# Kernel optimization log

Hardware: AMD Instinct MI355X
Metric: run time of the kernel (lower is better)

## Reference

```python
import jax, jax.numpy as jnp
import numpy as np

D_MODEL = 2048
HEADS = 16
HEAD_DIM = D_MODEL // HEADS
INNER = 8192
SEQ = 2048
EPS = 1e-5


def _layernorm(x, g, b):
    mu = jnp.mean(x, axis=-1, keepdims=True)
    var = jnp.mean(jnp.square(x - mu), axis=-1, keepdims=True)
    return (x - mu) * jax.lax.rsqrt(var + EPS) * g + b


def setup_inputs() -> dict:
    key = jax.random.key(0)
    ks = jax.random.split(key, 10)
    s = 0.02
    return {
        "x": jax.random.normal(ks[0], (1, SEQ, D_MODEL), dtype=jnp.float32),
        "C_w": jax.random.normal(ks[1], (D_MODEL, 3 * D_MODEL), dtype=jnp.float32) * s,
        "C_b": jnp.zeros((3 * D_MODEL,), dtype=jnp.float32),
        "lin_w": jax.random.normal(ks[2], (D_MODEL, D_MODEL), dtype=jnp.float32) * s,
        "lin_b": jnp.zeros((D_MODEL,), dtype=jnp.float32),
        "ff1_w": jax.random.normal(ks[3], (D_MODEL, INNER), dtype=jnp.float32) * s,
        "ff1_b": jnp.zeros((INNER,), dtype=jnp.float32),
        "ff2_w": jax.random.normal(ks[4], (INNER, D_MODEL), dtype=jnp.float32) * s,
        "ff2_b": jnp.zeros((D_MODEL,), dtype=jnp.float32),
        "ln1_g": jnp.ones((D_MODEL,), dtype=jnp.float32),
        "ln1_b": jnp.zeros((D_MODEL,), dtype=jnp.float32),
        "ln2_g": jnp.ones((D_MODEL,), dtype=jnp.float32),
        "ln2_b": jnp.zeros((D_MODEL,), dtype=jnp.float32),
    }


def reference(x, C_w, C_b, lin_w, lin_b, ff1_w, ff1_b, ff2_w, ff2_b,
              ln1_g, ln1_b, ln2_g, ln2_b):
    b, s, d = x.shape
    c = x @ C_w + C_b                       # [b, s, 3d]
    q, k, v = jnp.split(c, 3, axis=2)
    q = q.reshape(b, s, HEADS, HEAD_DIM)
    k = k.reshape(b, s, HEADS, HEAD_DIM)
    v = v.reshape(b, s, HEADS, HEAD_DIM)
    # NOTE: source scales by sqrt(d_model), NOT sqrt(head_dim)
    qk = jnp.einsum('bqhd,bkhd->bhqk', q, k) / jnp.sqrt(jnp.float32(d))
    causal = jnp.tril(jnp.ones((s, s), dtype=bool))  # [s, s]
    qk = jnp.where(causal[None, None, :, :], qk, -jnp.inf)
    scores = jax.nn.softmax(qk, axis=3)
    out = jnp.einsum('bhqk,bkhd->bqhd', scores, v).reshape(b, s, d)
    attn = out @ lin_w + lin_b
    h1 = _layernorm(x + attn, ln1_g, ln1_b)
    ff = jax.nn.gelu(h1 @ ff1_w + ff1_b, approximate=False) @ ff2_w + ff2_b
    return _layernorm(h1 + ff, ln2_g, ln2_b)
```

## Files before the change

### kernel.cpp

```cpp
#include <hip/hip_runtime.h>
#include <hip/hip_bf16.h>

#define SEQ 2048
#define DM 2048
#define NH 16
#define HD 128
#define FF 8192

typedef float f4v __attribute__((ext_vector_type(4)));
typedef short s8v __attribute__((ext_vector_type(8)));

__device__ __forceinline__ ushort f2bf(float f) {
  unsigned int x = __float_as_uint(f);
  unsigned int r = (x + 0x7FFFu + ((x >> 16) & 1u)) >> 16;
  return (ushort)r;
}

#define AS1 __attribute__((address_space(1)))
#define AS3 __attribute__((address_space(3)))
__device__ __forceinline__ void load16_lds(const ushort* g, ushort* l) {
  __builtin_amdgcn_global_load_lds((const AS1 unsigned int*)g, (AS3 unsigned int*)l, 16, 0, 0);
}

__global__ __launch_bounds__(256) void k_cvt(const float* __restrict__ in,
                                             ushort* __restrict__ out, int n4) {
  int i = blockIdx.x * 256 + threadIdx.x;
  if (i >= n4) return;
  f4v v = reinterpret_cast<const f4v*>(in)[i];
  ushort4 u;
  u.x = f2bf(v[0]); u.y = f2bf(v[1]); u.z = f2bf(v[2]); u.w = f2bf(v[3]);
  reinterpret_cast<ushort4*>(out)[i] = u;
}

__global__ __launch_bounds__(256) void k_tr(const float* __restrict__ W,
                                            ushort* __restrict__ Wt,
                                            int K, int N) {
  __shared__ float tile[32][36];
  int t = threadIdx.x;
  int n0 = blockIdx.x * 32, k0 = blockIdx.y * 32;
  int lr = t >> 3, lc = (t & 7) * 4;
  *(f4v*)&tile[lr][lc] = *(const f4v*)&W[(size_t)(k0 + lr) * N + n0 + lc];
  __syncthreads();
  int sn = t >> 3, sk = (t & 7) * 4;
  ushort4 u;
  u.x = f2bf(tile[sk + 0][sn]);
  u.y = f2bf(tile[sk + 1][sn]);
  u.z = f2bf(tile[sk + 2][sn]);
  u.w = f2bf(tile[sk + 3][sn]);
  *(ushort4*)&Wt[(size_t)(n0 + sn) * K + k0 + sk] = u;
}

__global__ __launch_bounds__(256) void k_gemm(const ushort* __restrict__ A,
                                              const ushort* __restrict__ Bt,
                                              const float* __restrict__ bias,
                                              float* __restrict__ Cf,
                                              ushort* __restrict__ Cb,
                                              int M, int N, int K, int gelu) {
  __shared__ ushort As[128 * 64];
  __shared__ ushort Bs[128 * 64];
  const int m0 = blockIdx.y * 128, n0 = blockIdx.x * 128;
  const int t = threadIdx.x;
  const int wave = t >> 6, lane = t & 63;
  const int wm = (wave >> 1) * 64, wn = (wave & 1) * 64;
  const int quad = lane >> 4, l16 = lane & 15;
  f4v acc[4][4] = {};
  const int srow = lane >> 3;
  const int scg = (lane & 7) ^ srow;
  const ushort* gA = A + (size_t)(m0 + wave * 32 + srow) * K + scg * 8;
  const ushort* gB = Bt + (size_t)(n0 + wave * 32 + srow) * K + scg * 8;
  ushort* lA = &As[(wave * 32 + srow - srow) * 64];
  ushort* lB = &Bs[(wave * 32) * 64];
  lA = &As[(wave * 32) * 64];

  for (int k0 = 0; k0 < K; k0 += 64) {
#pragma unroll
    for (int p = 0; p < 4; ++p) {
      load16_lds(gA + (size_t)p * 8 * K + k0, lA + p * 8 * 64);
      load16_lds(gB + (size_t)p * 8 * K + k0, lB + p * 8 * 64);
    }
    __syncthreads();
#pragma unroll
    for (int kk = 0; kk < 64; kk += 32) {
      s8v af[4], bf[4];
#pragma unroll
      for (int i = 0; i < 4; ++i) {
        int ar = wm + i * 16 + l16;
        af[i] = *(const s8v*)&As[ar * 64 + ((((kk >> 3) + quad) ^ (ar & 7)) * 8)];
      }
#pragma unroll
      for (int j = 0; j < 4; ++j) {
        int br = wn + j * 16 + l16;
        bf[j] = *(const s8v*)&Bs[br * 64 + ((((kk >> 3) + quad) ^ (br & 7)) * 8)];
      }
#pragma unroll
      for (int i = 0; i < 4; ++i)
#pragma unroll
        for (int j = 0; j < 4; ++j)
          acc[i][j] = __builtin_amdgcn_mfma_f32_16x16x32_bf16(af[i], bf[j], acc[i][j], 0, 0, 0);
    }
    __syncthreads();
  }
#pragma unroll
  for (int i = 0; i < 4; ++i) {
    int rbase = m0 + wm + i * 16 + quad * 4;
#pragma unroll
    for (int j = 0; j < 4; ++j) {
      int cidx = n0 + wn + j * 16 + l16;
      float b = bias[cidx];
#pragma unroll
      for (int r = 0; r < 4; ++r) {
        float v = acc[i][j][r] + b;
        if (gelu) v = 0.5f * v * (1.0f + erff(v * 0.70710678118654752f));
        if (Cf) Cf[(size_t)(rbase + r) * N + cidx] = v;
        if (Cb) Cb[(size_t)(rbase + r) * N + cidx] = f2bf(v);
      }
    }
  }
}

__global__ __launch_bounds__(256) void k_attn_mfma(const ushort* __restrict__ qkv,
                                                   ushort* __restrict__ ctx) {
  __shared__ ushort Ks[64][136];
  __shared__ ushort Vt[128][72];
  __shared__ ushort Ps[4][16][72];
  const int idx = blockIdx.x;
  const int h = idx & (NH - 1);
  const int qt = (SEQ / 64 - 1) - (idx >> 4);
  const int q0 = qt * 64;
  const int t = threadIdx.x;
  const int wave = t >> 6, lane = t & 63;
  const int quad = lane >> 4, l16 = lane & 15;
  const float scale = 0.022097086912079608f;

  s8v aq[4];
  {
    const ushort* qp = qkv + (size_t)(q0 + 16 * wave + l16) * (3 * DM) + h * HD + quad * 8;
#pragma unroll
    for (int ks = 0; ks < 4; ++ks)
      aq[ks] = *(const s8v*)(qp + ks * 32);
  }
  f4v acc_o[8] = {};
  float m_r[4], l_r[4];
#pragma unroll
  for (int r = 0; r < 4; ++r) { m_r[r] = -1e30f; l_r[r] = 0.0f; }

  for (int kt = 0; kt <= qt; ++kt) {
    const int k0 = kt * 64;
    __syncthreads();
    {
      const ushort* kp = qkv + (size_t)k0 * (3 * DM) + DM + h * HD;
#pragma unroll
      for (int i = 0; i < 4; ++i) {
        int ch = t + i * 256;
        int row = ch >> 4, c8 = (ch & 15) * 8;
        *(s8v*)&Ks[row][c8] = *(const s8v*)(kp + (size_t)row * (3 * DM) + c8);
      }
      const ushort* vp = qkv + (size_t)k0 * (3 * DM) + 2 * DM + h * HD;
#pragma unroll
      for (int i = 0; i < 4; ++i) {
        int id = t + i * 256;
        int d = id & 127, sg = id >> 7;
        ushort e0 = vp[(size_t)(sg * 8 + 0) * (3 * DM) + d];
        ushort e1 = vp[(size_t)(sg * 8 + 1) * (3 * DM) + d];
        ushort e2 = vp[(size_t)(sg * 8 + 2) * (3 * DM) + d];
        ushort e3 = vp[(size_t)(sg * 8 + 3) * (3 * DM) + d];
        ushort e4 = vp[(size_t)(sg * 8 + 4) * (3 * DM) + d];
        ushort e5 = vp[(size_t)(sg * 8 + 5) * (3 * DM) + d];
        ushort e6 = vp[(size_t)(sg * 8 + 6) * (3 * DM) + d];
        ushort e7 = vp[(size_t)(sg * 8 + 7) * (3 * DM) + d];
        uint4 pk;
        pk.x = (uint)e0 | ((uint)e1 << 16);
        pk.y = (uint)e2 | ((uint)e3 << 16);
        pk.z = (uint)e4 | ((uint)e5 << 16);
        pk.w = (uint)e6 | ((uint)e7 << 16);
        *(uint4*)&Vt[d][sg * 8] = pk;
      }
    }
    __syncthreads();

    f4v sacc[4] = {};
#pragma unroll
    for (int ks = 0; ks < 4; ++ks) {
      s8v bk[4];
#pragma unroll
      for (int j = 0; j < 4; ++j)
        bk[j] = *(const s8v*)&Ks[j * 16 + l16][ks * 32 + quad * 8];
#pragma unroll
      for (int j = 0; j < 4; ++j)
        sacc[j] = __builtin_amdgcn_mfma_f32_16x16x32_bf16(aq[ks], bk[j], sacc[j], 0, 0, 0);
    }
    if (kt == qt) {
#pragma unroll
      for (int j = 0; j < 4; ++j)
#pragma unroll
        for (int r = 0; r < 4; ++r) {
          int lrow = 16 * wave + quad * 4 + r;
          int lcol = j * 16 + l16;
          sacc[j][r] = (lcol > lrow) ? -1e30f : sacc[j][r] * scale;
        }
    } else {
#pragma unroll
      for (int j = 0; j < 4; ++j)
#pragma unroll
        for (int r = 0; r < 4; ++r) sacc[j][r] *= scale;
    }
    float alpha[4];
#pragma unroll
    for (int r = 0; r < 4; ++r) {
      float mx = fmaxf(fmaxf(sacc[0][r], sacc[1][r]), fmaxf(sacc[2][r], sacc[3][r]));
      mx = fmaxf(mx, __shfl_xor(mx, 1));
      mx = fmaxf(mx, __shfl_xor(mx, 2));
      mx = fmaxf(mx, __shfl_xor(mx, 4));
      mx = fmaxf(mx, __shfl_xor(mx, 8));
      float mn = fmaxf(m_r[r], mx);
      alpha[r] = __expf(m_r[r] - mn);
      m_r[r] = mn;
      float ps = 0.0f;
#pragma unroll
      for (int j = 0; j < 4; ++j) {
        float p = __expf(sacc[j][r] - mn);
        sacc[j][r] = p;
        ps += p;
      }
      ps += __shfl_xor(ps, 1);
      ps += __shfl_xor(ps, 2);
      ps += __shfl_xor(ps, 4);
      ps += __shfl_xor(ps, 8);
      l_r[r] = l_r[r] * alpha[r] + ps;
    }
#pragma unroll
    for (int j = 0; j < 4; ++j)
#pragma unroll
      for (int r = 0; r < 4; ++r)
        Ps[wave][quad * 4 + r][j * 16 + l16] = f2bf(sacc[j][r]);
#pragma unroll
    for (int nd = 0; nd < 8; ++nd)
#pragma unroll
      for (int r = 0; r < 4; ++r) acc_o[nd][r] *= alpha[r];
#pragma unroll
    for (int ks2 = 0; ks2 < 2; ++ks2) {
      s8v ap = *(const s8v*)&Ps[wave][l16][ks2 * 32 + quad * 8];
#pragma unroll
      for (int nd = 0; nd < 8; ++nd) {
        s8v bv = *(const s8v*)&Vt[nd * 16 + l16][ks2 * 32 + quad * 8];
        acc_o[nd] = __builtin_amdgcn_mfma_f32_16x16x32_bf16(ap, bv, acc_o[nd], 0, 0, 0);
      }
    }
  }
  float rl[4];
#pragma unroll
  for (int r = 0; r < 4; ++r) rl[r] = 1.0f / l_r[r];
#pragma unroll
  for (int nd = 0; nd < 8; ++nd) {
    int col = h * HD + nd * 16 + l16;
#pragma unroll
    for (int r = 0; r < 4; ++r) {
      int row = q0 + 16 * wave + quad * 4 + r;
      ctx[(size_t)row * DM + col] = f2bf(acc_o[nd][r] * rl[r]);
    }
  }
}

__global__ __launch_bounds__(256) void k_ln(const float* __restrict__ A,
                                            const float* __restrict__ B,
                                            const float* __restrict__ g,
                                            const float* __restrict__ be,
                                            float* __restrict__ outf,
                                            ushort* __restrict__ outb) {
  int row = blockIdx.x;
  int t = threadIdx.x;
  const f4v* av = reinterpret_cast<const f4v*>(A + (size_t)row * DM);
  const f4v* bv = reinterpret_cast<const f4v*>(B + (size_t)row * DM);
  f4v x0 = av[t] + bv[t];
  f4v x1 = av[t + 256] + bv[t + 256];
  float s = x0[0] + x0[1] + x0[2] + x0[3] + x1[0] + x1[1] + x1[2] + x1[3];
  float q = x0[0]*x0[0] + x0[1]*x0[1] + x0[2]*x0[2] + x0[3]*x0[3]
          + x1[0]*x1[0] + x1[1]*x1[1] + x1[2]*x1[2] + x1[3]*x1[3];
#pragma unroll
  for (int off = 32; off; off >>= 1) {
    s += __shfl_down(s, off, 64);
    q += __shfl_down(q, off, 64);
  }
  __shared__ float rs[4], rq[4];
  if ((t & 63) == 0) { rs[t >> 6] = s; rq[t >> 6] = q; }
  __syncthreads();
  s = rs[0] + rs[1] + rs[2] + rs[3];
  q = rq[0] + rq[1] + rq[2] + rq[3];
  float mu = s * (1.0f / DM);
  float var = q * (1.0f / DM) - mu * mu;
  float rstd = rsqrtf(var + 1e-5f);
  const f4v* gv = reinterpret_cast<const f4v*>(g);
  const f4v* bev = reinterpret_cast<const f4v*>(be);
  f4v y0 = (x0 - mu) * rstd * gv[t] + bev[t];
  f4v y1 = (x1 - mu) * rstd * gv[t + 256] + bev[t + 256];
  reinterpret_cast<f4v*>(outf + (size_t)row * DM)[t] = y0;
  reinterpret_cast<f4v*>(outf + (size_t)row * DM)[t + 256] = y1;
  if (outb) {
    ushort4 u0, u1;
    u0.x = f2bf(y0[0]); u0.y = f2bf(y0[1]); u0.z = f2bf(y0[2]); u0.w = f2bf(y0[3]);
    u1.x = f2bf(y1[0]); u1.y = f2bf(y1[1]); u1.z = f2bf(y1[2]); u1.w = f2bf(y1[3]);
    reinterpret_cast<ushort4*>(outb + (size_t)row * DM)[t] = u0;
    reinterpret_cast<ushort4*>(outb + (size_t)row * DM)[t + 256] = u1;
  }
}

extern "C" void kernel_launch(void* const* d_in, const int* in_sizes, int n_in,
                              void* d_out, int out_size, void* d_ws, size_t ws_size,
                              hipStream_t stream) {
  const float* x     = (const float*)d_in[0];
  const float* C_w   = (const float*)d_in[1];
  const float* C_b   = (const float*)d_in[2];
  const float* lin_w = (const float*)d_in[3];
  const float* lin_b = (const float*)d_in[4];
  const float* ff1_w = (const float*)d_in[5];
  const float* ff1_b = (const float*)d_in[6];
  const float* ff2_w = (const float*)d_in[7];
  const float* ff2_b = (const float*)d_in[8];
  const float* ln1g  = (const float*)d_in[9];
  const float* ln1b  = (const float*)d_in[10];
  const float* ln2g  = (const float*)d_in[11];
  const float* ln2b  = (const float*)d_in[12];

  char* ws = (char*)d_ws;
  size_t off = 0;
  auto take = [&](size_t bytes) {
    char* p = ws + off;
    off += (bytes + 255) & ~(size_t)255;
    return p;
  };
  ushort* Wt   = (ushort*)take((size_t)FF * DM * 2);
  ushort* qkvb = (ushort*)take((size_t)SEQ * 3 * DM * 2);
  ushort* xb   = (ushort*)take((size_t)SEQ * DM * 2);
  ushort* ctxb = (ushort*)take((size_t)SEQ * DM * 2);
  ushort* bigb = (ushort*)take((size_t)SEQ * FF * 2);
  float*  attn = (float*) take((size_t)SEQ * DM * 4);
  float*  h1   = (float*) take((size_t)SEQ * DM * 4);
  float*  ff2o = (float*) take((size_t)SEQ * DM * 4);

  k_cvt<<<SEQ * DM / 1024, 256, 0, stream>>>(x, xb, SEQ * DM / 4);
  k_tr<<<dim3(3 * DM / 32, DM / 32), 256, 0, stream>>>(C_w, Wt, DM, 3 * DM);
  k_gemm<<<dim3(3 * DM / 128, SEQ / 128), 256, 0, stream>>>(xb, Wt, C_b, nullptr, qkvb, SEQ, 3 * DM, DM, 0);
  k_attn_mfma<<<dim3((SEQ / 64) * NH), 256, 0, stream>>>(qkvb, ctxb);
  k_tr<<<dim3(DM / 32, DM / 32), 256, 0, stream>>>(lin_w, Wt, DM, DM);
  k_gemm<<<dim3(DM / 128, SEQ / 128), 256, 0, stream>>>(ctxb, Wt, lin_b, attn, nullptr, SEQ, DM, DM, 0);
  k_ln<<<SEQ, 256, 0, stream>>>(x, attn, ln1g, ln1b, h1, xb);
  k_tr<<<dim3(FF / 32, DM / 32), 256, 0, stream>>>(ff1_w, Wt, DM, FF);
  k_gemm<<<dim3(FF / 128, SEQ / 128), 256, 0, stream>>>(xb, Wt, ff1_b, nullptr, bigb, SEQ, FF, DM, 1);
  k_tr<<<dim3(DM / 32, FF / 32), 256, 0, stream>>>(ff2_w, Wt, FF, DM);
  k_gemm<<<dim3(DM / 128, SEQ / 128), 256, 0, stream>>>(bigb, Wt, ff2_b, ff2o, nullptr, SEQ, DM, FF, 0);
  k_ln<<<SEQ, 256, 0, stream>>>(h1, ff2o, ln2g, ln2b, (float*)d_out, (ushort*)nullptr);
}
```

Baseline: 718.2 us.

## Split-K the N=2048 GEMMs and reduce partials inside layernorm

Adds a blockIdx.z K-split to the GEMM kernel so the out-projection and FF2 GEMMs launch four times as many blocks, each writing an fp32 partial slice. The layernorm kernel is extended to sum the four partials and add the bias before normalizing. This targets under-occupancy from only 256 output tiles, at the cost of extra partial-buffer writes and reads.

```diff
diff --git a/kernel.cpp b/kernel.cpp
--- a/kernel.cpp
+++ b/kernel.cpp
@@ -63,16 +63,18 @@
   const int wave = t >> 6, lane = t & 63;
   const int wm = (wave >> 1) * 64, wn = (wave & 1) * 64;
   const int quad = lane >> 4, l16 = lane & 15;
+  const int kchunk = K / gridDim.z;
+  const int kbeg = blockIdx.z * kchunk, kend = kbeg + kchunk;
+  if (Cf && gridDim.z > 1) Cf += (size_t)blockIdx.z * M * N;
   f4v acc[4][4] = {};
   const int srow = lane >> 3;
   const int scg = (lane & 7) ^ srow;
   const ushort* gA = A + (size_t)(m0 + wave * 32 + srow) * K + scg * 8;
   const ushort* gB = Bt + (size_t)(n0 + wave * 32 + srow) * K + scg * 8;
-  ushort* lA = &As[(wave * 32 + srow - srow) * 64];
+  ushort* lA = &As[(wave * 32) * 64];
   ushort* lB = &Bs[(wave * 32) * 64];
-  lA = &As[(wave * 32) * 64];
-
-  for (int k0 = 0; k0 < K; k0 += 64) {
+
+  for (int k0 = kbeg; k0 < kend; k0 += 64) {
 #pragma unroll
     for (int p = 0; p < 4; ++p) {
       load16_lds(gA + (size_t)p * 8 * K + k0, lA + p * 8 * 64);
@@ -106,7 +108,7 @@
 #pragma unroll
     for (int j = 0; j < 4; ++j) {
       int cidx = n0 + wn + j * 16 + l16;
-      float b = bias[cidx];
+      float b = bias ? bias[cidx] : 0.0f;
 #pragma unroll
       for (int r = 0; r < 4; ++r) {
         float v = acc[i][j][r] + b;
@@ -261,18 +263,26 @@
   }
 }
 
-__global__ __launch_bounds__(256) void k_ln(const float* __restrict__ A,
-                                            const float* __restrict__ B,
-                                            const float* __restrict__ g,
-                                            const float* __restrict__ be,
-                                            float* __restrict__ outf,
-                                            ushort* __restrict__ outb) {
+__global__ __launch_bounds__(256) void k_ln_sk(const float* __restrict__ A,
+                                               const float* __restrict__ P, int np,
+                                               const float* __restrict__ bias,
+                                               const float* __restrict__ g,
+                                               const float* __restrict__ be,
+                                               float* __restrict__ outf,
+                                               ushort* __restrict__ outb) {
   int row = blockIdx.x;
   int t = threadIdx.x;
   const f4v* av = reinterpret_cast<const f4v*>(A + (size_t)row * DM);
-  const f4v* bv = reinterpret_cast<const f4v*>(B + (size_t)row * DM);
-  f4v x0 = av[t] + bv[t];
-  f4v x1 = av[t + 256] + bv[t + 256];
+  f4v x0 = av[t];
+  f4v x1 = av[t + 256];
+  for (int s = 0; s < np; ++s) {
+    const f4v* pv = reinterpret_cast<const f4v*>(P + (size_t)s * SEQ * DM + (size_t)row * DM);
+    x0 += pv[t];
+    x1 += pv[t + 256];
+  }
+  const f4v* bb = reinterpret_cast<const f4v*>(bias);
+  x0 += bb[t];
+  x1 += bb[t + 256];
   float s = x0[0] + x0[1] + x0[2] + x0[3] + x1[0] + x1[1] + x1[2] + x1[3];
   float q = x0[0]*x0[0] + x0[1]*x0[1] + x0[2]*x0[2] + x0[3]*x0[3]
           + x1[0]*x1[0] + x1[1]*x1[1] + x1[2]*x1[2] + x1[3]*x1[3];
@@ -333,20 +343,19 @@
   ushort* xb   = (ushort*)take((size_t)SEQ * DM * 2);
   ushort* ctxb = (ushort*)take((size_t)SEQ * DM * 2);
   ushort* bigb = (ushort*)take((size_t)SEQ * FF * 2);
-  float*  attn = (float*) take((size_t)SEQ * DM * 4);
   float*  h1   = (float*) take((size_t)SEQ * DM * 4);
-  float*  ff2o = (float*) take((size_t)SEQ * DM * 4);
+  float*  part = (float*) take((size_t)4 * SEQ * DM * 4);
 
   k_cvt<<<SEQ * DM / 1024, 256, 0, stream>>>(x, xb, SEQ * DM / 4);
   k_tr<<<dim3(3 * DM / 32, DM / 32), 256, 0, stream>>>(C_w, Wt, DM, 3 * DM);
-  k_gemm<<<dim3(3 * DM / 128, SEQ / 128), 256, 0, stream>>>(xb, Wt, C_b, nullptr, qkvb, SEQ, 3 * DM, DM, 0);
+  k_gemm<<<dim3(3 * DM / 128, SEQ / 128, 1), 256, 0, stream>>>(xb, Wt, C_b, nullptr, qkvb, SEQ, 3 * DM, DM, 0);
   k_attn_mfma<<<dim3((SEQ / 64) * NH), 256, 0, stream>>>(qkvb, ctxb);
   k_tr<<<dim3(DM / 32, DM / 32), 256, 0, stream>>>(lin_w, Wt, DM, DM);
-  k_gemm<<<dim3(DM / 128, SEQ / 128), 256, 0, stream>>>(ctxb, Wt, lin_b, attn, nullptr, SEQ, DM, DM, 0);
-  k_ln<<<SEQ, 256, 0, stream>>>(x, attn, ln1g, ln1b, h1, xb);
+  k_gemm<<<dim3(DM / 128, SEQ / 128, 4), 256, 0, stream>>>(ctxb, Wt, nullptr, part, nullptr, SEQ, DM, DM, 0);
+  k_ln_sk<<<SEQ, 256, 0, stream>>>(x, part, 4, lin_b, ln1g, ln1b, h1, xb);
   k_tr<<<dim3(FF / 32, DM / 32), 256, 0, stream>>>(ff1_w, Wt, DM, FF);
-  k_gemm<<<dim3(FF / 128, SEQ / 128), 256, 0, stream>>>(xb, Wt, ff1_b, nullptr, bigb, SEQ, FF, DM, 1);
+  k_gemm<<<dim3(FF / 128, SEQ / 128, 1), 256, 0, stream>>>(xb, Wt, ff1_b, nullptr, bigb, SEQ, FF, DM, 1);
   k_tr<<<dim3(DM / 32, FF / 32), 256, 0, stream>>>(ff2_w, Wt, FF, DM);
-  k_gemm<<<dim3(DM / 128, SEQ / 128), 256, 0, stream>>>(bigb, Wt, ff2_b, ff2o, nullptr, SEQ, DM, FF, 0);
-  k_ln<<<SEQ, 256, 0, stream>>>(h1, ff2o, ln2g, ln2b, (float*)d_out, (ushort*)nullptr);
-}
+  k_gemm<<<dim3(DM / 128, SEQ / 128, 4), 256, 0, stream>>>(bigb, Wt, nullptr, part, nullptr, SEQ, DM, FF, 0);
+  k_ln_sk<<<SEQ, 256, 0, stream>>>(h1, part, 4, ff2_b, ln2g, ln2b, (float*)d_out, (ushort*)nullptr);
+}
```

Result: faster. 651.8 us (-9.2%).
